# Kernel optimization log

Hardware: AMD Instinct MI355X
Metric: run time of the kernel (lower is better)

Reference implementation:

```python
import jax, jax.numpy as jnp
import numpy as np

EPS = 1e-5
NUM_HEADS = 8
TOP_K = 4

def _ln(x, s, b):
    m = x.mean(-1, keepdims=True)
    v = ((x - m) ** 2).mean(-1, keepdims=True)
    return (x - m) / jnp.sqrt(v + EPS) * s + b

def _mha(x, wq, bq, wk, bk, wv, bv, wo, bo):
    B, S, D = x.shape
    dh = D // NUM_HEADS
    q = (x @ wq + bq).reshape(B, S, NUM_HEADS, dh)
    k = (x @ wk + bk).reshape(B, S, NUM_HEADS, dh)
    v = (x @ wv + bv).reshape(B, S, NUM_HEADS, dh)
    att = jnp.einsum('bqhd,bkhd->bhqk', q, k) / np.sqrt(dh).astype(x.dtype)
    a = jax.nn.softmax(att, axis=-1)
    o = jnp.einsum('bhqk,bkhd->bqhd', a, v).reshape(B, S, D)
    return o @ wo + bo

def _moe(x, rd, ru, w1, b1, w2, b2, ws1, bs1, ws2, bs2):
    B, S, D = x.shape
    N = B * S
    E = ru.shape[-1]
    t = x.reshape(N, D)
    scores = (t @ rd) @ ru                       # [N,E] low-rank router
    probs = jax.nn.softmax(scores, axis=-1)
    tv, ti = jax.lax.top_k(probs, TOP_K)          # [N,K]
    tw = tv / tv.sum(-1, keepdims=True)           # renormalized gate weights
    oh = jax.nn.one_hot(ti, E, dtype=t.dtype)     # [N,K,E]
    gates = (oh * tw[..., None]).sum(1)           # sparse [N,E] combine weights
    h = jax.nn.gelu(jnp.einsum('nd,edh->enh', t, w1) + b1[:, None, :])
    eo = jnp.einsum('enh,ehd->end', h, w2) + b2[:, None, :]
    routed = jnp.einsum('end,ne->nd', eo, gates)
    shared = jax.nn.gelu(t @ ws1 + bs1) @ ws2 + bs2
    out = (routed + shared).reshape(B, S, D)
    # aux losses: load-balance + router z-loss
    f = oh.sum(1).mean(0)                         # mean assignments per expert
    P = probs.mean(0)
    lb = (E / TOP_K) * jnp.sum(f * P)
    z = jnp.mean(jax.nn.logsumexp(scores, axis=-1) ** 2)
    return out, lb, z

def reference(x, ln1_s, ln1_b, ln2_s, ln2_b, wq, bq, wk, bk, wv, bv, wo, bo,
              router_down, router_up, w1, b1, w2, b2, ws1, bs1, ws2, bs2, fn_s, fn_b):
    L = wq.shape[0]
    lbs, zs = [], []
    for l in range(L):
        x = x + _mha(_ln(x, ln1_s[l], ln1_b[l]), wq[l], bq[l], wk[l], bk[l],
                     wv[l], bv[l], wo[l], bo[l])
        moe_out, lb, z = _moe(_ln(x, ln2_s[l], ln2_b[l]), router_down[l], router_up[l],
                              w1[l], b1[l], w2[l], b2[l], ws1[l], bs1[l], ws2[l], bs2[l])
        x = x + moe_out
        lbs.append(lb)
        zs.append(z)
    x = _ln(x, fn_s, fn_b)
    return x, jnp.stack(lbs), jnp.stack(zs)

def setup_inputs() -> dict:
    key = jax.random.key(0)
    ks = jax.random.split(key, 16)
    L, D, E, R, H, HS, B, S = 2, 512, 32, 64, 512, 4096, 4, 1024
    w = 0.02  # init scale for weights
    return {
        'x': jax.random.normal(ks[0], (B, S, D), jnp.float32),
        'ln1_s': jnp.ones((L, D)), 'ln1_b': jnp.zeros((L, D)),
        'ln2_s': jnp.ones((L, D)), 'ln2_b': jnp.zeros((L, D)),
        'wq': jax.random.normal(ks[1], (L, D, D)) * w, 'bq': jnp.zeros((L, D)),
        'wk': jax.random.normal(ks[2], (L, D, D)) * w, 'bk': jnp.zeros((L, D)),
        'wv': jax.random.normal(ks[3], (L, D, D)) * w, 'bv': jnp.zeros((L, D)),
        'wo': jax.random.normal(ks[4], (L, D, D)) * w, 'bo': jnp.zeros((L, D)),
        'router_down': jax.random.normal(ks[5], (L, D, R)) * w,
        'router_up': jax.random.normal(ks[6], (L, R, E)) * w,
        'w1': jax.random.normal(ks[7], (L, E, D, H)) * w, 'b1': jnp.zeros((L, E, H)),
        'w2': jax.random.normal(ks[8], (L, E, H, D)) * w, 'b2': jnp.zeros((L, E, D)),
        'ws1': jax.random.normal(ks[9], (L, D, HS)) * w, 'bs1': jnp.zeros((L, HS)),
        'ws2': jax.random.normal(ks[10], (L, HS, D)) * w, 'bs2': jnp.zeros((L, D)),
        'fn_s': jnp.ones((D,)), 'fn_b': jnp.zeros((D,)),
    }
```

## Files before the change

### kernel.cpp

```cpp
#include <hip/hip_runtime.h>
#include <math.h>

#define NTOK    4096
#define DMODEL  512
#define NEXP    32
#define RRANK   64
#define HEXP    512
#define HSHARED 4096
#define SEQ     1024
#define BATCH   4
#define NHEAD   8
#define TOPK    4
#define NLAYER  2
#define QBLK    64
#define KBLK    64
#define MAXTILE 160
#define DDU     262144

typedef __attribute__((ext_vector_type(8))) short bf16x8;
typedef __attribute__((ext_vector_type(4))) float f32x4;

__device__ __forceinline__ float gelu_f(float x) {
    float t = tanhf(0.7978845608028654f * (x + 0.044715f * x * x * x));
    return 0.5f * x * (1.f + t);
}
__device__ __forceinline__ unsigned short f2bf(float f) {
    unsigned int u = __float_as_uint(f);
    u += 0x7FFFu + ((u >> 16) & 1u);
    return (unsigned short)(u >> 16);
}
__device__ __forceinline__ float bf2f(unsigned short u) {
    return __uint_as_float((unsigned int)u << 16);
}
__device__ __forceinline__ void gl_lds16(const void* g, void* l) {
    __builtin_amdgcn_global_load_lds(
        (const __attribute__((address_space(1))) void*)g,
        (__attribute__((address_space(3))) void*)l, 16, 0, 0);
}

template <int MODE>
__global__ __launch_bounds__(256) void ln_kernel(const float* __restrict__ x,
                                                 const float* __restrict__ s,
                                                 const float* __restrict__ b,
                                                 float* __restrict__ outf,
                                                 unsigned short* __restrict__ outb) {
    int wave = threadIdx.x >> 6, lane = threadIdx.x & 63;
    int row = blockIdx.x * 4 + wave;
    const float* xr = x + (size_t)row * DMODEL;
    float v[8];
    float sum = 0.f;
#pragma unroll
    for (int i = 0; i < 8; i++) { v[i] = xr[lane + i * 64]; sum += v[i]; }
#pragma unroll
    for (int o = 32; o; o >>= 1) sum += __shfl_xor(sum, o);
    float m = sum * (1.f / DMODEL);
    float vs = 0.f;
#pragma unroll
    for (int i = 0; i < 8; i++) { float d = v[i] - m; vs += d * d; }
#pragma unroll
    for (int o = 32; o; o >>= 1) vs += __shfl_xor(vs, o);
    float rstd = rsqrtf(vs * (1.f / DMODEL) + 1e-5f);
#pragma unroll
    for (int i = 0; i < 8; i++) {
        int c = lane + i * 64;
        float r = (v[i] - m) * rstd * s[c] + b[c];
        if (MODE != 1) outf[(size_t)row * DMODEL + c] = r;
        if (MODE != 0) outb[(size_t)row * DMODEL + c] = f2bf(r);
    }
}

template <int SK, bool MOE, int MODE, bool ROUTER = false>
__global__ __launch_bounds__(256) void reduceln_kernel(
    const float* __restrict__ pbuf, const float* __restrict__ bias,
    const unsigned short* __restrict__ eogb, const float* __restrict__ topw,
    const int* __restrict__ pos, float* __restrict__ xb,
    const float* __restrict__ s, const float* __restrict__ b,
    float* __restrict__ outf, unsigned short* __restrict__ outb,
    const float* __restrict__ rdru, float* __restrict__ rsc) {
    int wave = threadIdx.x >> 6, lane = threadIdx.x & 63;
    int row = blockIdx.x * 4 + wave;
    int cb = lane * 8;
    size_t base = (size_t)row * DMODEL + cb;
    float v[8];
    {
        float4 a0 = *(const float4*)(xb + base);
        float4 a1 = *(const float4*)(xb + base + 4);
        float4 b0 = *(const float4*)(bias + cb);
        float4 b1 = *(const float4*)(bias + cb + 4);
        v[0] = a0.x + b0.x; v[1] = a0.y + b0.y; v[2] = a0.z + b0.z; v[3] = a0.w + b0.w;
        v[4] = a1.x + b1.x; v[5] = a1.y + b1.y; v[6] = a1.z + b1.z; v[7] = a1.w + b1.w;
    }
#pragma unroll
    for (int sk = 0; sk < SK; sk++) {
        const float* p = pbuf + (size_t)sk * NTOK * DMODEL + base;
        float4 p0 = *(const float4*)p;
        float4 p1 = *(const float4*)(p + 4);
        v[0] += p0.x; v[1] += p0.y; v[2] += p0.z; v[3] += p0.w;
        v[4] += p1.x; v[5] += p1.y; v[6] += p1.z; v[7] += p1.w;
    }
    if (MOE) {
#pragma unroll
        for (int k = 0; k < TOPK; k++) {
            float w = topw[row * TOPK + k];
            bf16x8 e = *(const bf16x8*)(eogb + (size_t)pos[row * TOPK + k] * DMODEL + cb);
#pragma unroll
            for (int i = 0; i < 8; i++) v[i] += w * bf2f((unsigned short)e[i]);
        }
    }
    *(float4*)(xb + base) = make_float4(v[0], v[1], v[2], v[3]);
    *(float4*)(xb + base + 4) = make_float4(v[4], v[5], v[6], v[7]);
    float sum = 0.f;
#pragma unroll
    for (int i = 0; i < 8; i++) sum += v[i];
#pragma unroll
    for (int o = 32; o; o >>= 1) sum += __shfl_xor(sum, o);
    float m = sum * (1.f / DMODEL);
    float vs = 0.f;
#pragma unroll
    for (int i = 0; i < 8; i++) { float d = v[i] - m; vs += d * d; }
#pragma unroll
    for (int o = 32; o; o >>= 1) vs += __shfl_xor(vs, o);
    float rstd = rsqrtf(vs * (1.f / DMODEL) + 1e-5f);
    float rr[8];
#pragma unroll
    for (int i = 0; i < 8; i++) {
        int c = cb + i;
        rr[i] = (v[i] - m) * rstd * s[c] + b[c];
        if (MODE != 1) outf[(size_t)row * DMODEL + c] = rr[i];
        if (MODE != 0) outb[(size_t)row * DMODEL + c] = f2bf(rr[i]);
    }
    if (ROUTER) {
        float sc[NEXP];
#pragma unroll
        for (int e = 0; e < NEXP; e++) sc[e] = 0.f;
#pragma unroll
        for (int i = 0; i < 8; i++) {
            const float4* rp = (const float4*)(rdru + (size_t)(cb + i) * NEXP);
            float rv = rr[i];
#pragma unroll
            for (int e4 = 0; e4 < 8; e4++) {
                float4 q = rp[e4];
                sc[e4 * 4 + 0] += rv * q.x;
                sc[e4 * 4 + 1] += rv * q.y;
                sc[e4 * 4 + 2] += rv * q.z;
                sc[e4 * 4 + 3] += rv * q.w;
            }
        }
#pragma unroll
        for (int e = 0; e < NEXP; e++) {
#pragma unroll
            for (int o = 32; o; o >>= 1) sc[e] += __shfl_xor(sc[e], o);
        }
        if (lane == 0) {
            float* rp = rsc + (size_t)row * NEXP;
#pragma unroll
            for (int e = 0; e < NEXP; e++) rp[e] = sc[e];
        }
    }
}

__global__ __launch_bounds__(256) void wtall_kernel(
    const float* __restrict__ wq, const float* __restrict__ wk,
    const float* __restrict__ wv, const float* __restrict__ wo,
    const float* __restrict__ w1, const float* __restrict__ w2,
    const float* __restrict__ ws1, const float* __restrict__ ws2,
    const float* __restrict__ bq, const float* __restrict__ bk, const float* __restrict__ bv,
    unsigned short* __restrict__ wqkvt, unsigned short* __restrict__ wot,
    unsigned short* __restrict__ w1t, unsigned short* __restrict__ w2t,
    unsigned short* __restrict__ ws1t, unsigned short* __restrict__ ws2t,
    float* __restrict__ bqkv, int* __restrict__ stats) {
    __shared__ float tbuf[64][68];
    int bkid = blockIdx.x;
    int tid = threadIdx.x;
    if (bkid >= 5376) {
        int i = (bkid - 5376) * 256 + tid;
        float val = (i < 512) ? bq[i] : (i < 1024 ? bk[i - 512] : bv[i - 1024]);
        bqkv[i] = val;
        if (i < 160) stats[i] = 0;
        return;
    }
    const float* src;
    unsigned short* dst;
    int K, N, tx, ty;
    if (bkid < 256) {
        int w = bkid >> 6, t = bkid & 63;
        K = 512; N = 512; ty = t >> 3; tx = t & 7;
        if (w == 0)      { src = wq; dst = wqkvt; }
        else if (w == 1) { src = wk; dst = wqkvt + DDU; }
        else if (w == 2) { src = wv; dst = wqkvt + 2 * (size_t)DDU; }
        else             { src = wo; dst = wot; }
    } else if (bkid < 2304) {
        int t = bkid - 256; int e = t >> 6; int tt = t & 63;
        K = 512; N = 512; ty = tt >> 3; tx = tt & 7;
        src = w1 + (size_t)e * DDU; dst = w1t + (size_t)e * DDU;
    } else if (bkid < 4352) {
        int t = bkid - 2304; int e = t >> 6; int tt = t & 63;
        K = 512; N = 512; ty = tt >> 3; tx = tt & 7;
        src = w2 + (size_t)e * DDU; dst = w2t + (size_t)e * DDU;
    } else if (bkid < 4864) {
        int t = bkid - 4352;
        K = 512; N = 4096; tx = t & 63; ty = t >> 6;
        src = ws1; dst = ws1t;
    } else {
        int t = bkid - 4864;
        K = 4096; N = 512; tx = t & 7; ty = t >> 3;
        src = ws2; dst = ws2t;
    }
    int k0 = ty * 64, n0 = tx * 64;
    int r = tid >> 2, cb4 = (tid & 3) * 4;
#pragma unroll
    for (int i = 0; i < 4; i++)
        *(float4*)&tbuf[r][cb4 + i * 16] = *(const float4*)(src + (size_t)(k0 + r) * N + n0 + cb4 + i * 16);
    __syncthreads();
    int g = tid & 7, nr = tid >> 3;
#pragma unroll
    for (int i = 0; i < 2; i++) {
        int n = nr + i * 32;
        bf16x8 v;
#pragma unroll
        for (int j = 0; j < 8; j++) v[j] = (short)f2bf(tbuf[g * 8 + j][n]);
        *(bf16x8*)(dst + (size_t)(n0 + n) * K + k0 + g * 8) = v;
    }
}

__global__ __launch_bounds__(256) void vtr_kernel(const unsigned short* __restrict__ QKV,
                                                  unsigned short* __restrict__ Vt) {
    int st = blockIdx.x, hh = blockIdx.y, bb = blockIdx.z;
    __shared__ unsigned short t[64][72];
    int r = threadIdx.x >> 3, g = threadIdx.x & 7;
#pragma unroll
    for (int i = 0; i < 2; i++) {
        int row = r + i * 32;
        bf16x8 v = *(const bf16x8*)(QKV + (size_t)(bb * SEQ + st * 64 + row) * 1536 + 1024 + hh * 64 + g * 8);
        *(bf16x8*)&t[row][g * 8] = v;
    }
    __syncthreads();
#pragma unroll
    for (int i = 0; i < 2; i++) {
        int d = r + i * 32;
        bf16x8 v;
#pragma unroll
        for (int j = 0; j < 8; j++) v[j] = (short)t[g * 8 + j][d];
        *(bf16x8*)(Vt + (size_t)((bb * NHEAD + hh) * 64 + d) * SEQ + st * 64 + g * 8) = v;
    }
}

template <bool GELU, bool DORES, bool GATHER, bool EXPERT, bool OUTBF16, int SK = 1, int BK = 64>
__global__ __launch_bounds__(256, 2) void gemm_mfma(
    const unsigned short* __restrict__ Ab, const unsigned short* __restrict__ Wt,
    const float* __restrict__ bias, const float* __restrict__ res,
    void* __restrict__ Cvoid, int M, int Nn, int Kk,
    const int* __restrict__ rowmap, const int* __restrict__ cntp,
    const int* __restrict__ offp, const int* __restrict__ tinfo) {
    constexpr int RS  = BK * 2;
    constexpr int CH  = RS / 16;
    constexpr int RPI = 1024 / RS;
    constexpr int AIW = 32 / RPI;
    constexpr int BIW = 16 / RPI;
    unsigned int bid = blockIdx.y * gridDim.x + blockIdx.x;
    unsigned int tot = gridDim.x * gridDim.y;
    unsigned int lg = (bid & 7) * (tot >> 3) + (bid >> 3);
    unsigned int bx = lg % gridDim.x;
    unsigned int by = lg / gridDim.x;
    int n0 = bx * 64;
    int m0;
    size_t cbase = 0;
    int kbeg = 0, kend = Kk;
    if (EXPERT) {
        int t = by;
        if (t >= tinfo[0]) return;
        int e = tinfo[1 + 2 * t];
        m0 = tinfo[2 + 2 * t];
        M = cntp[e];
        Wt += (size_t)e * Nn * Kk;
        bias += (size_t)e * Nn;
        int oe = offp[e];
        cbase = (size_t)oe * Nn;
        if (GATHER) rowmap += oe;
        else Ab += (size_t)oe * Kk;
    } else {
        m0 = by * 128;
    }
    if (SK > 1) {
        int s = blockIdx.z;
        int chunk = Kk / SK;
        kbeg = s * chunk;
        kend = kbeg + chunk;
        cbase = (size_t)s * M * Nn;
    }
    __shared__ short As[128 * BK];
    __shared__ short Bs[64 * BK];
    char* asb = (char*)As;
    char* bsb = (char*)Bs;
    int tid = threadIdx.x;
    int wave = tid >> 6, lane = tid & 63;
    int wm = wave >> 1, wn = wave & 1;
    int l15 = lane & 15, l16 = lane >> 4;
    int c16 = lane & (CH - 1);
    int ro  = lane / CH;

    const char* aptr[AIW];
    const char* bptr[BIW];
#pragma unroll
    for (int j = 0; j < AIW; j++) {
        int rloc = j * RPI + ro;
        int row = wave * 32 + rloc;
        int grow = m0 + row;
        int arow = GATHER ? rowmap[grow] : grow;
        int srcoff = ((c16 ^ (rloc & (CH - 1))) << 4);
        aptr[j] = (const char*)Ab + (((size_t)arow * Kk) << 1) + srcoff;
    }
#pragma unroll
    for (int j = 0; j < BIW; j++) {
        int rloc = j * RPI + ro;
        int row = wave * 16 + rloc;
        int srcoff = ((c16 ^ (rloc & (CH - 1))) << 4);
        bptr[j] = (const char*)Wt + (((size_t)(n0 + row) * Kk) << 1) + srcoff;
    }

    f32x4 acc[4][2];
#pragma unroll
    for (int m = 0; m < 4; m++)
#pragma unroll
        for (int n = 0; n < 2; n++)
#pragma unroll
            for (int j = 0; j < 4; j++) acc[m][n][j] = 0.f;

    for (int k0 = kbeg; k0 < kend; k0 += BK) {
        size_t kb = (size_t)k0 << 1;
#pragma unroll
        for (int j = 0; j < AIW; j++) gl_lds16(aptr[j] + kb, asb + wave * 32 * RS + j * 1024);
#pragma unroll
        for (int j = 0; j < BIW; j++) gl_lds16(bptr[j] + kb, bsb + wave * 16 * RS + j * 1024);
        __syncthreads();
#pragma unroll
        for (int kk = 0; kk < BK / 32; kk++) {
            int k8 = kk * 4 + l16;
            bf16x8 a[4], b[2];
#pragma unroll
            for (int m = 0; m < 4; m++) {
                int row = wm * 64 + m * 16 + l15;
                a[m] = *(const bf16x8*)(asb + row * RS + ((k8 * 16) ^ ((row & (CH - 1)) << 4)));
            }
#pragma unroll
            for (int n = 0; n < 2; n++) {
                int row = wn * 32 + n * 16 + l15;
                b[n] = *(const bf16x8*)(bsb + row * RS + ((k8 * 16) ^ ((row & (CH - 1)) << 4)));
            }
#pragma unroll
            for (int m = 0; m < 4; m++)
#pragma unroll
                for (int n = 0; n < 2; n++)
                    acc[m][n] = __builtin_amdgcn_mfma_f32_16x16x32_bf16(a[m], b[n], acc[m][n], 0, 0, 0);
        }
        __syncthreads();
    }

#pragma unroll
    for (int m = 0; m < 4; m++) {
#pragma unroll
        for (int n = 0; n < 2; n++) {
            int col = n0 + wn * 32 + n * 16 + l15;
            float bv = (SK == 1 && bias) ? bias[col] : 0.f;
#pragma unroll
            for (int j = 0; j < 4; j++) {
                int row = m0 + wm * 64 + m * 16 + l16 * 4 + j;
                if (row >= M) continue;
                float val = acc[m][n][j] + bv;
                if (SK == 1 && GELU) val = gelu_f(val);
                if (SK == 1 && DORES) val += res[(size_t)row * Nn + col];
                if (SK == 1 && OUTBF16)
                    ((unsigned short*)Cvoid)[cbase + (size_t)row * Nn + col] = f2bf(val);
                else
                    ((float*)Cvoid)[cbase + (size_t)row * Nn + col] = val;
            }
        }
    }
}

template <bool GELU>
__global__ __launch_bounds__(256) void gemm_tile(
    const float* __restrict__ A, const float* __restrict__ W,
    float* __restrict__ C, int M, int Nn, int Kk, int lda) {
    int n0 = blockIdx.x * 64;
    int m0 = blockIdx.y * 64;
    __shared__ float Asf[16][68];
    __shared__ float Wsf[16][68];
    int tid = threadIdx.x;
    int ml = tid >> 2, kl = (tid & 3) << 2;
    bool avalid = (m0 + ml) < M;
    int arow = m0 + ml;
    const float* aptr = A + (size_t)arow * lda + kl;
    int kr = tid >> 4, nc = (tid & 15) << 2;
    bool wvalid = (n0 + nc) < Nn;
    const float* wptr = W + (size_t)kr * Nn + n0 + nc;
    int tm = (tid >> 4) << 2, tn = (tid & 15) << 2;
    float acc[4][4] = {{0.f}};
    for (int k0 = 0; k0 < Kk; k0 += 16) {
        float4 av = make_float4(0.f, 0.f, 0.f, 0.f);
        float4 wv = make_float4(0.f, 0.f, 0.f, 0.f);
        if (avalid) av = *(const float4*)(aptr + k0);
        if (wvalid) wv = *(const float4*)(wptr + (size_t)k0 * Nn);
        Asf[kl + 0][ml] = av.x; Asf[kl + 1][ml] = av.y;
        Asf[kl + 2][ml] = av.z; Asf[kl + 3][ml] = av.w;
        *(float4*)&Wsf[kr][nc] = wv;
        __syncthreads();
#pragma unroll
        for (int kk = 0; kk < 16; kk++) {
            float4 a4 = *(const float4*)&Asf[kk][tm];
            float4 w4 = *(const float4*)&Wsf[kk][tn];
            acc[0][0] += a4.x * w4.x; acc[0][1] += a4.x * w4.y; acc[0][2] += a4.x * w4.z; acc[0][3] += a4.x * w4.w;
            acc[1][0] += a4.y * w4.x; acc[1][1] += a4.y * w4.y; acc[1][2] += a4.y * w4.z; acc[1][3] += a4.y * w4.w;
            acc[2][0] += a4.z * w4.x; acc[2][1] += a4.z * w4.y; acc[2][2] += a4.z * w4.z; acc[2][3] += a4.z * w4.w;
            acc[3][0] += a4.w * w4.x; acc[3][1] += a4.w * w4.y; acc[3][2] += a4.w * w4.z; acc[3][3] += a4.w * w4.w;
        }
        __syncthreads();
    }
#pragma unroll
    for (int i = 0; i < 4; i++) {
        int mm = m0 + tm + i;
        if (mm >= M) break;
        float* crow = C + (size_t)mm * Nn;
#pragma unroll
        for (int j = 0; j < 4; j++) {
            int nn = n0 + tn + j;
            if (nn >= Nn) continue;
            float val = acc[i][j];
            if (GELU) val = gelu_f(val);
            crow[nn] = val;
        }
    }
}

__global__ __launch_bounds__(256, 2) void attn_mfma(const unsigned short* __restrict__ QKV,
                                                    const unsigned short* __restrict__ Vt,
                                                    unsigned short* __restrict__ O) {
    int qt = blockIdx.x, hh = blockIdx.y, bb = blockIdx.z;
    __shared__ char lds[32768];
    char* Qs = lds;
    char* Ks = lds + 8192;
    char* Vs = lds + 16384;
    char* Ps = lds + 24576;
    int tid = threadIdx.x;
    int w = tid >> 6, l = tid & 63;
    int l15 = l & 15, l16 = l >> 4;

    {
        int r = tid >> 3, g = tid & 7;
        const unsigned short* qbase = QKV + (size_t)(bb * SEQ + qt * QBLK) * 1536 + hh * 64;
#pragma unroll
        for (int i = 0; i < 2; i++) {
            int row = r + i * 32;
            bf16x8 v = *(const bf16x8*)(qbase + (size_t)row * 1536 + g * 8);
            *(bf16x8*)(Qs + row * 128 + ((g * 16) ^ ((row & 7) << 4))) = v;
        }
    }
    f32x4 accO[4];
#pragma unroll
    for (int n = 0; n < 4; n++)
#pragma unroll
        for (int j = 0; j < 4; j++) accO[n][j] = 0.f;
    float m_r[4] = {-1e30f, -1e30f, -1e30f, -1e30f};
    float l_r[4] = {0.f, 0.f, 0.f, 0.f};

    const unsigned short* kbase = QKV + (size_t)(bb * SEQ) * 1536 + 512 + hh * 64;
    const unsigned short* vbase = Vt + (size_t)((bb * NHEAD + hh) * 64) * SEQ;

    for (int kt = 0; kt < SEQ / KBLK; kt++) {
        __syncthreads();
        {
            int r = tid >> 3, g = tid & 7;
#pragma unroll
            for (int i = 0; i < 2; i++) {
                int row = r + i * 32;
                bf16x8 kv = *(const bf16x8*)(kbase + (size_t)(kt * KBLK + row) * 1536 + g * 8);
                *(bf16x8*)(Ks + row * 128 + ((g * 16) ^ ((row & 7) << 4))) = kv;
                bf16x8 vv = *(const bf16x8*)(vbase + (size_t)row * SEQ + kt * KBLK + g * 8);
                *(bf16x8*)(Vs + row * 128 + ((g * 16) ^ ((row & 7) << 4))) = vv;
            }
        }
        __syncthreads();
        f32x4 s_acc[4];
#pragma unroll
        for (int n = 0; n < 4; n++)
#pragma unroll
            for (int j = 0; j < 4; j++) s_acc[n][j] = 0.f;
#pragma unroll
        for (int st = 0; st < 2; st++) {
            int kb = st * 64 + l16 * 16;
            int qrow = w * 16 + l15;
            bf16x8 a = *(const bf16x8*)(Qs + qrow * 128 + (kb ^ ((qrow & 7) << 4)));
#pragma unroll
            for (int n = 0; n < 4; n++) {
                int kr = n * 16 + l15;
                bf16x8 b = *(const bf16x8*)(Ks + kr * 128 + (kb ^ ((kr & 7) << 4)));
                s_acc[n] = __builtin_amdgcn_mfma_f32_16x16x32_bf16(a, b, s_acc[n], 0, 0, 0);
            }
        }
        char* pw = Ps + w * 2048;
#pragma unroll
        for (int j = 0; j < 4; j++) {
            float s0 = s_acc[0][j] * 0.125f, s1 = s_acc[1][j] * 0.125f;
            float s2 = s_acc[2][j] * 0.125f, s3 = s_acc[3][j] * 0.125f;
            float tmax = fmaxf(fmaxf(s0, s1), fmaxf(s2, s3));
#pragma unroll
            for (int o = 1; o < 16; o <<= 1) tmax = fmaxf(tmax, __shfl_xor(tmax, o));
            float mnew = fmaxf(m_r[j], tmax);
            float resc = __expf(m_r[j] - mnew);
            float p0 = __expf(s0 - mnew), p1 = __expf(s1 - mnew);
            float p2 = __expf(s2 - mnew), p3 = __expf(s3 - mnew);
            float ps = p0 + p1 + p2 + p3;
#pragma unroll
            for (int o = 1; o < 16; o <<= 1) ps += __shfl_xor(ps, o);
            l_r[j] = l_r[j] * resc + ps;
            m_r[j] = mnew;
            accO[0][j] *= resc; accO[1][j] *= resc;
            accO[2][j] *= resc; accO[3][j] *= resc;
            int prow = l16 * 4 + j;
            int sw = (prow & 7) << 4;
            *(unsigned short*)(pw + prow * 128 + ((2 * l15) ^ sw)) = f2bf(p0);
            *(unsigned short*)(pw + prow * 128 + ((2 * l15 + 32) ^ sw)) = f2bf(p1);
            *(unsigned short*)(pw + prow * 128 + ((2 * l15 + 64) ^ sw)) = f2bf(p2);
            *(unsigned short*)(pw + prow * 128 + ((2 * l15 + 96) ^ sw)) = f2bf(p3);
        }
#pragma unroll
        for (int st = 0; st < 2; st++) {
            int kb = st * 64 + l16 * 16;
            bf16x8 pa = *(const bf16x8*)(pw + l15 * 128 + (kb ^ ((l15 & 7) << 4)));
#pragma unroll
            for (int n = 0; n < 4; n++) {
                int vr = n * 16 + l15;
                bf16x8 vb = *(const bf16x8*)(Vs + vr * 128 + (kb ^ ((vr & 7) << 4)));
                accO[n] = __builtin_amdgcn_mfma_f32_16x16x32_bf16(pa, vb, accO[n], 0, 0, 0);
            }
        }
    }
    unsigned short* obase = O + (size_t)(bb * SEQ + qt * QBLK + w * 16) * DMODEL + hh * 64;
#pragma unroll
    for (int j = 0; j < 4; j++) {
        float inv = 1.f / l_r[j];
        int row = l16 * 4 + j;
#pragma unroll
        for (int n = 0; n < 4; n++)
            obase[(size_t)row * DMODEL + n * 16 + l15] = f2bf(accO[n][j] * inv);
    }
}

__global__ __launch_bounds__(256) void router_topk(const float* __restrict__ rsc,
                                                   float* __restrict__ topw,
                                                   int* __restrict__ topi,
                                                   int* __restrict__ cnt,
                                                   float* __restrict__ sumP,
                                                   float* __restrict__ zacc) {
    __shared__ float wP[4][NEXP];
    __shared__ int wC[4][NEXP];
    __shared__ float wZ[4];
    int tid = threadIdx.x;
    int wv = tid >> 6, lane = tid & 63;
    int n = blockIdx.x * 256 + tid;
    float sc[NEXP];
    float mx = -1e30f;
#pragma unroll
    for (int e = 0; e < NEXP; e++) { sc[e] = rsc[n * NEXP + e]; mx = fmaxf(mx, sc[e]); }
    float se = 0.f;
#pragma unroll
    for (int e = 0; e < NEXP; e++) { sc[e] = expf(sc[e] - mx); se += sc[e]; }
    float invse = 1.f / se;
    float lse = mx + logf(se);
    float z = lse * lse;
#pragma unroll
    for (int o = 32; o; o >>= 1) z += __shfl_xor(z, o);
    if (lane == 0) wZ[wv] = z;
#pragma unroll
    for (int e = 0; e < NEXP; e++) {
        float pv = sc[e] * invse;
#pragma unroll
        for (int o = 32; o; o >>= 1) pv += __shfl_xor(pv, o);
        if (lane == 0) wP[wv][e] = pv;
    }
    float tv[TOPK]; int ti[TOPK];
#pragma unroll
    for (int k = 0; k < TOPK; k++) {
        float best = -1.f; int bi = 0;
#pragma unroll
        for (int e = 0; e < NEXP; e++) {
            if (sc[e] > best) { best = sc[e]; bi = e; }
        }
        tv[k] = best * invse; ti[k] = bi; sc[bi] = -1.f;
    }
    float s4 = tv[0] + tv[1] + tv[2] + tv[3];
#pragma unroll
    for (int k = 0; k < TOPK; k++) {
        topw[n * TOPK + k] = tv[k] / s4;
        topi[n * TOPK + k] = ti[k];
    }
#pragma unroll
    for (int e = 0; e < NEXP; e++) {
        unsigned long long b0 = __ballot(ti[0] == e);
        unsigned long long b1 = __ballot(ti[1] == e);
        unsigned long long b2 = __ballot(ti[2] == e);
        unsigned long long b3 = __ballot(ti[3] == e);
        if (lane == 0)
            wC[wv][e] = __popcll(b0) + __popcll(b1) + __popcll(b2) + __popcll(b3);
    }
    __syncthreads();
    if (tid < NEXP) {
        atomicAdd(&sumP[tid], wP[0][tid] + wP[1][tid] + wP[2][tid] + wP[3][tid]);
        atomicAdd(&cnt[tid], wC[0][tid] + wC[1][tid] + wC[2][tid] + wC[3][tid]);
    }
    if (tid == 0) atomicAdd(zacc, wZ[0] + wZ[1] + wZ[2] + wZ[3]);
}

__global__ void scanaux_kernel(const int* __restrict__ cnt, int* __restrict__ poff,
                               int* __restrict__ tinfo, int* __restrict__ perm,
                               const float* __restrict__ sumP, const float* __restrict__ zacc,
                               float* __restrict__ out_aux, int l) {
    int lane = threadIdx.x;
    int c = (lane < NEXP) ? cnt[lane] : 0;
    int nt = (c + 127) >> 7;
    int x = nt;
#pragma unroll
    for (int o = 1; o < 32; o <<= 1) {
        int y = __shfl_up(x, o);
        if (lane >= o) x += y;
    }
    int excl = x - nt;
    if (lane < NEXP) {
        poff[lane] = excl * 128;
        for (int i = 0; i < nt; i++) {
            tinfo[1 + 2 * (excl + i)] = lane;
            tinfo[2 + 2 * (excl + i)] = i * 128;
        }
        for (int i = c; i < nt * 128; i++) perm[excl * 128 + i] = 0;
    }
    float lb = (lane < NEXP) ? ((float)c / (float)NTOK) * (sumP[lane] / (float)NTOK) : 0.f;
#pragma unroll
    for (int o = 32; o; o >>= 1) lb += __shfl_xor(lb, o);
    if (lane == 31) {
        tinfo[0] = x;
        out_aux[l] = lb * (float)NEXP / (float)TOPK;
        out_aux[NLAYER + l] = zacc[0] / (float)NTOK;
    }
}

__global__ __launch_bounds__(256) void scatter_kernel(const int* __restrict__ topi,
                                                      const int* __restrict__ poff,
                                                      int* __restrict__ cursor,
                                                      int* __restrict__ perm,
                                                      int* __restrict__ pos) {
    __shared__ int lcnt[NEXP];
    __shared__ int lbase[NEXP];
    if (threadIdx.x < NEXP) lcnt[threadIdx.x] = 0;
    __syncthreads();
    int i = blockIdx.x * 256 + threadIdx.x;
    int e = topi[i];
    int lr = atomicAdd(&lcnt[e], 1);
    __syncthreads();
    if (threadIdx.x < NEXP && lcnt[threadIdx.x] > 0)
        lbase[threadIdx.x] = atomicAdd(&cursor[threadIdx.x], lcnt[threadIdx.x]);
    __syncthreads();
    int g = poff[e] + lbase[e] + lr;
    perm[g] = i >> 2;
    pos[i] = g;
}

extern "C" void kernel_launch(void* const* d_in, const int* in_sizes, int n_in,
                              void* d_out, int out_size, void* d_ws, size_t ws_size,
                              hipStream_t stream) {
    (void)in_sizes; (void)n_in; (void)out_size; (void)ws_size;
    const float* x_in  = (const float*)d_in[0];
    const float* ln1_s = (const float*)d_in[1];
    const float* ln1_b = (const float*)d_in[2];
    const float* ln2_s = (const float*)d_in[3];
    const float* ln2_b = (const float*)d_in[4];
    const float* wq = (const float*)d_in[5];
    const float* bq = (const float*)d_in[6];
    const float* wk = (const float*)d_in[7];
    const float* bk = (const float*)d_in[8];
    const float* wv = (const float*)d_in[9];
    const float* bv = (const float*)d_in[10];
    const float* wo = (const float*)d_in[11];
    const float* bo = (const float*)d_in[12];
    const float* rdw = (const float*)d_in[13];
    const float* ruw = (const float*)d_in[14];
    const float* w1 = (const float*)d_in[15];
    const float* b1 = (const float*)d_in[16];
    const float* w2 = (const float*)d_in[17];
    const float* b2 = (const float*)d_in[18];
    const float* ws1 = (const float*)d_in[19];
    const float* bs1 = (const float*)d_in[20];
    const float* ws2 = (const float*)d_in[21];
    const float* bs2 = (const float*)d_in[22];
    const float* fn_s = (const float*)d_in[23];
    const float* fn_b = (const float*)d_in[24];

    float* ws = (float*)d_ws;
    const size_t ND = (size_t)NTOK * DMODEL;
    const size_t PADROWS = (size_t)MAXTILE * 128;
    size_t o = 0;
    float* xb  = ws + o; o += ND;
    unsigned short* hb     = (unsigned short*)(ws + o); o += ND / 2;
    unsigned short* qkv_bf = (unsigned short*)(ws + o); o += (size_t)NTOK * 1536 / 2;
    unsigned short* vT     = (unsigned short*)(ws + o); o += ND / 2;
    unsigned short* t1b    = (unsigned short*)(ws + o); o += ND / 2;
    unsigned short* hidb   = (unsigned short*)(ws + o); o += (size_t)NTOK * HSHARED / 2;
    unsigned short* eogb   = (unsigned short*)(ws + o); o += PADROWS * DMODEL / 2;
    float* pbuf = ws + o; o += 4 * ND;
    float* rdru = ws + o; o += (size_t)DMODEL * NEXP;
    float* rsc  = ws + o; o += (size_t)NTOK * NEXP;
    float* topw = ws + o; o += (size_t)NTOK * TOPK;
    float* bqkv = ws + o; o += 1536;
    int* topi = (int*)(ws + o); o += (size_t)NTOK * TOPK;
    int* pos  = (int*)(ws + o); o += (size_t)NTOK * TOPK;
    int* perm = (int*)(ws + o); o += PADROWS;
    int* stats = (int*)(ws + o); o += 256;
    int* tinfo = (int*)(ws + o); o += 512;
    int* cnt = stats;
    int* cursor = stats + 32;
    int* poff = stats + 64;
    float* sumP = (float*)(stats + 96);
    float* zacc = sumP + 32;
    unsigned short* wbf = (unsigned short*)(ws + o);
    unsigned short* wqkvt = wbf;
    unsigned short* wot  = wqkvt + 3 * (size_t)DDU;
    unsigned short* w1t  = wot + DDU;
    unsigned short* w2t  = w1t + (size_t)NEXP * DDU;
    unsigned short* ws1t = w2t + (size_t)NEXP * DDU;
    unsigned short* ws2t = ws1t + (size_t)DMODEL * HSHARED;

    float* out_x = (float*)d_out;
    float* out_aux = out_x + ND;

    hipMemcpyAsync(xb, x_in, ND * sizeof(float), hipMemcpyDeviceToDevice, stream);

    dim3 blk(256);
    dim3 gQKV(1536 / 64, NTOK / 128);
    dim3 gOP(DMODEL / 64, NTOK / 128, 2);
    dim3 gF2(DMODEL / 64, NTOK / 128, 4);
    dim3 gHS(HSHARED / 64, NTOK / 128);
    dim3 gE1(HEXP / 64, MAXTILE);
    dim3 gE2(DMODEL / 64, MAXTILE);

    for (int l = 0; l < NLAYER; l++) {
        const size_t DD = (size_t)DMODEL * DMODEL;
        wtall_kernel<<<5382, blk, 0, stream>>>(
            wq + l * DD, wk + l * DD, wv + l * DD, wo + l * DD,
            w1 + (size_t)l * NEXP * DD, w2 + (size_t)l * NEXP * DD,
            ws1 + (size_t)l * DMODEL * HSHARED, ws2 + (size_t)l * HSHARED * DMODEL,
            bq + l * DMODEL, bk + l * DMODEL, bv + l * DMODEL,
            wqkvt, wot, w1t, w2t, ws1t, ws2t, bqkv, stats);
        gemm_tile<false><<<dim3(1, 8), blk, 0, stream>>>(
            rdw + (size_t)l * DMODEL * RRANK, ruw + (size_t)l * RRANK * NEXP, rdru, DMODEL, NEXP, RRANK, RRANK);

        if (l == 0)
            ln_kernel<1><<<NTOK / 4, blk, 0, stream>>>(xb, ln1_s, ln1_b, nullptr, hb);
        gemm_mfma<false, false, false, false, true><<<gQKV, blk, 0, stream>>>(
            hb, wqkvt, bqkv, nullptr, qkv_bf, NTOK, 1536, DMODEL, nullptr, nullptr, nullptr, nullptr);
        vtr_kernel<<<dim3(SEQ / 64, NHEAD, BATCH), blk, 0, stream>>>(qkv_bf, vT);
        attn_mfma<<<dim3(SEQ / QBLK, NHEAD, BATCH), blk, 0, stream>>>(qkv_bf, vT, t1b);
        gemm_mfma<false, false, false, false, false, 2><<<gOP, blk, 0, stream>>>(
            t1b, wot, nullptr, nullptr, pbuf, NTOK, DMODEL, DMODEL, nullptr, nullptr, nullptr, nullptr);
        reduceln_kernel<2, false, 1, true><<<NTOK / 4, blk, 0, stream>>>(
            pbuf, bo + l * DMODEL, nullptr, nullptr, nullptr, xb,
            ln2_s + l * DMODEL, ln2_b + l * DMODEL, nullptr, hb, rdru, rsc);
        router_topk<<<NTOK / 256, blk, 0, stream>>>(rsc, topw, topi, cnt, sumP, zacc);
        scanaux_kernel<<<1, 64, 0, stream>>>(cnt, poff, tinfo, perm, sumP, zacc, out_aux, l);
        scatter_kernel<<<NTOK * TOPK / 256, blk, 0, stream>>>(topi, poff, cursor, perm, pos);
        gemm_mfma<true, false, true, true, true><<<gE1, blk, 0, stream>>>(
            hb, w1t, b1 + (size_t)l * NEXP * HEXP, nullptr,
            hidb, 0, HEXP, DMODEL, perm, cnt, poff, tinfo);
        gemm_mfma<false, false, false, true, true><<<gE2, blk, 0, stream>>>(
            hidb, w2t, b2 + (size_t)l * NEXP * DMODEL, nullptr,
            eogb, 0, DMODEL, HEXP, nullptr, cnt, poff, tinfo);
        gemm_mfma<true, false, false, false, true><<<gHS, blk, 0, stream>>>(
            hb, ws1t, bs1 + (size_t)l * HSHARED, nullptr,
            hidb, NTOK, HSHARED, DMODEL, nullptr, nullptr, nullptr, nullptr);
        gemm_mfma<false, false, false, false, false, 4><<<gF2, blk, 0, stream>>>(
            hidb, ws2t, nullptr, nullptr, pbuf, NTOK, DMODEL, HSHARED, nullptr, nullptr, nullptr, nullptr);
        if (l + 1 < NLAYER) {
            reduceln_kernel<4, true, 1, false><<<NTOK / 4, blk, 0, stream>>>(
                pbuf, bs2 + l * DMODEL, eogb, topw, pos, xb,
                ln1_s + (l + 1) * DMODEL, ln1_b + (l + 1) * DMODEL, nullptr, hb, nullptr, nullptr);
        } else {
            reduceln_kernel<4, true, 0, false><<<NTOK / 4, blk, 0, stream>>>(
                pbuf, bs2 + l * DMODEL, eogb, topw, pos, xb,
                fn_s, fn_b, out_x, nullptr, nullptr, nullptr);
        }
    }
}
```

Before: 566.9 us.

## Merge shared and routed expert GEMMs into combined MLP1/MLP2 launches

Factors the MFMA GEMM into a device body and adds two kernels that each run the shared-expert GEMM and the routed-expert GEMM in one grid, split by block index. This cuts four launches per layer to two and lets the small, tile-count-dependent expert GEMMs fill the GPU alongside the large shared GEMMs, so there are fewer tail-underutilization gaps. A separate ehid buffer is added so the expert hidden activations no longer alias the shared hidden buffer. Expert blocks with no tile exit early, which can leave idle slots in the combined grid.

```diff
diff --git a/kernel.cpp b/kernel.cpp
--- a/kernel.cpp
+++ b/kernel.cpp
@@ -245,23 +245,21 @@
     }
 }
 
-template <bool GELU, bool DORES, bool GATHER, bool EXPERT, bool OUTBF16, int SK = 1, int BK = 64>
-__global__ __launch_bounds__(256, 2) void gemm_mfma(
-    const unsigned short* __restrict__ Ab, const unsigned short* __restrict__ Wt,
-    const float* __restrict__ bias, const float* __restrict__ res,
-    void* __restrict__ Cvoid, int M, int Nn, int Kk,
-    const int* __restrict__ rowmap, const int* __restrict__ cntp,
-    const int* __restrict__ offp, const int* __restrict__ tinfo) {
-    constexpr int RS  = BK * 2;
-    constexpr int CH  = RS / 16;
-    constexpr int RPI = 1024 / RS;
-    constexpr int AIW = 32 / RPI;
-    constexpr int BIW = 16 / RPI;
-    unsigned int bid = blockIdx.y * gridDim.x + blockIdx.x;
-    unsigned int tot = gridDim.x * gridDim.y;
-    unsigned int lg = (bid & 7) * (tot >> 3) + (bid >> 3);
-    unsigned int bx = lg % gridDim.x;
-    unsigned int by = lg / gridDim.x;
+template <bool GELU, bool GATHER, bool EXPERT, bool OUTBF16, int SK>
+__device__ __forceinline__ void gemm_body(
+    char* asb, char* bsb,
+    unsigned int rb, unsigned int gx, unsigned int tot, int zidx,
+    const unsigned short* Ab, const unsigned short* Wt,
+    const float* bias, void* Cvoid, int M, int Nn, int Kk,
+    const int* rowmap, const int* cntp, const int* offp, const int* tinfo) {
+    constexpr int RS  = 128;
+    constexpr int CH  = 8;
+    constexpr int RPI = 8;
+    constexpr int AIW = 4;
+    constexpr int BIW = 2;
+    unsigned int lg = (rb & 7) * (tot >> 3) + (rb >> 3);
+    unsigned int bx = lg % gx;
+    unsigned int by = lg / gx;
     int n0 = bx * 64;
     int m0;
     size_t cbase = 0;
@@ -282,16 +280,11 @@
         m0 = by * 128;
     }
     if (SK > 1) {
-        int s = blockIdx.z;
         int chunk = Kk / SK;
-        kbeg = s * chunk;
+        kbeg = zidx * chunk;
         kend = kbeg + chunk;
-        cbase = (size_t)s * M * Nn;
-    }
-    __shared__ short As[128 * BK];
-    __shared__ short Bs[64 * BK];
-    char* asb = (char*)As;
-    char* bsb = (char*)Bs;
+        cbase = (size_t)zidx * M * Nn;
+    }
     int tid = threadIdx.x;
     int wave = tid >> 6, lane = tid & 63;
     int wm = wave >> 1, wn = wave & 1;
@@ -326,7 +319,7 @@
 #pragma unroll
             for (int j = 0; j < 4; j++) acc[m][n][j] = 0.f;
 
-    for (int k0 = kbeg; k0 < kend; k0 += BK) {
+    for (int k0 = kbeg; k0 < kend; k0 += 64) {
         size_t kb = (size_t)k0 << 1;
 #pragma unroll
         for (int j = 0; j < AIW; j++) gl_lds16(aptr[j] + kb, asb + wave * 32 * RS + j * 1024);
@@ -334,7 +327,7 @@
         for (int j = 0; j < BIW; j++) gl_lds16(bptr[j] + kb, bsb + wave * 16 * RS + j * 1024);
         __syncthreads();
 #pragma unroll
-        for (int kk = 0; kk < BK / 32; kk++) {
+        for (int kk = 0; kk < 2; kk++) {
             int k8 = kk * 4 + l16;
             bf16x8 a[4], b[2];
 #pragma unroll
@@ -368,13 +361,72 @@
                 if (row >= M) continue;
                 float val = acc[m][n][j] + bv;
                 if (SK == 1 && GELU) val = gelu_f(val);
-                if (SK == 1 && DORES) val += res[(size_t)row * Nn + col];
                 if (SK == 1 && OUTBF16)
                     ((unsigned short*)Cvoid)[cbase + (size_t)row * Nn + col] = f2bf(val);
                 else
                     ((float*)Cvoid)[cbase + (size_t)row * Nn + col] = val;
             }
         }
+    }
+}
+
+template <bool GELU, bool GATHER, bool EXPERT, bool OUTBF16, int SK = 1>
+__global__ __launch_bounds__(256, 2) void gemm_mfma(
+    const unsigned short* __restrict__ Ab, const unsigned short* __restrict__ Wt,
+    const float* __restrict__ bias, void* __restrict__ Cvoid,
+    int M, int Nn, int Kk,
+    const int* __restrict__ rowmap, const int* __restrict__ cntp,
+    const int* __restrict__ offp, const int* __restrict__ tinfo) {
+    __shared__ short As[128 * 64];
+    __shared__ short Bs[64 * 64];
+    gemm_body<GELU, GATHER, EXPERT, OUTBF16, SK>(
+        (char*)As, (char*)Bs,
+        blockIdx.y * gridDim.x + blockIdx.x, gridDim.x, gridDim.x * gridDim.y, blockIdx.z,
+        Ab, Wt, bias, Cvoid, M, Nn, Kk, rowmap, cntp, offp, tinfo);
+}
+
+__global__ __launch_bounds__(256, 2) void mlp1_kernel(
+    const unsigned short* __restrict__ hb,
+    const unsigned short* __restrict__ ws1t, const float* __restrict__ bs1,
+    unsigned short* __restrict__ hidb,
+    const unsigned short* __restrict__ w1t, const float* __restrict__ b1,
+    unsigned short* __restrict__ ehid,
+    const int* __restrict__ perm, const int* __restrict__ cnt,
+    const int* __restrict__ poff, const int* __restrict__ tinfo) {
+    __shared__ short As[128 * 64];
+    __shared__ short Bs[64 * 64];
+    unsigned int bid = blockIdx.x;
+    if (bid < 2048) {
+        gemm_body<true, false, false, true, 1>(
+            (char*)As, (char*)Bs, bid, 64, 2048, 0,
+            hb, ws1t, bs1, hidb, NTOK, HSHARED, DMODEL, nullptr, nullptr, nullptr, nullptr);
+    } else {
+        gemm_body<true, true, true, true, 1>(
+            (char*)As, (char*)Bs, bid - 2048, 8, 1280, 0,
+            hb, w1t, b1, ehid, 0, HEXP, DMODEL, perm, cnt, poff, tinfo);
+    }
+}
+
+__global__ __launch_bounds__(256, 2) void mlp2_kernel(
+    const unsigned short* __restrict__ hidb,
+    const unsigned short* __restrict__ ws2t, float* __restrict__ pbuf,
+    const unsigned short* __restrict__ ehid,
+    const unsigned short* __restrict__ w2t, const float* __restrict__ b2,
+    unsigned short* __restrict__ eogb,
+    const int* __restrict__ cnt, const int* __restrict__ poff,
+    const int* __restrict__ tinfo) {
+    __shared__ short As[128 * 64];
+    __shared__ short Bs[64 * 64];
+    unsigned int bid = blockIdx.x;
+    if (bid < 1024) {
+        int zidx = bid >> 8;
+        gemm_body<false, false, false, false, 4>(
+            (char*)As, (char*)Bs, bid & 255, 8, 256, zidx,
+            hidb, ws2t, nullptr, pbuf, NTOK, DMODEL, HSHARED, nullptr, nullptr, nullptr, nullptr);
+    } else {
+        gemm_body<false, false, true, true, 1>(
+            (char*)As, (char*)Bs, bid - 1024, 8, 1280, 0,
+            ehid, w2t, b2, eogb, 0, DMODEL, HEXP, nullptr, cnt, poff, tinfo);
     }
 }
 
@@ -704,6 +756,7 @@
     unsigned short* vT     = (unsigned short*)(ws + o); o += ND / 2;
     unsigned short* t1b    = (unsigned short*)(ws + o); o += ND / 2;
     unsigned short* hidb   = (unsigned short*)(ws + o); o += (size_t)NTOK * HSHARED / 2;
+    unsigned short* ehid   = (unsigned short*)(ws + o); o += PADROWS * HEXP / 2;
     unsigned short* eogb   = (unsigned short*)(ws + o); o += PADROWS * DMODEL / 2;
     float* pbuf = ws + o; o += 4 * ND;
     float* rdru = ws + o; o += (size_t)DMODEL * NEXP;
@@ -736,10 +789,6 @@
     dim3 blk(256);
     dim3 gQKV(1536 / 64, NTOK / 128);
     dim3 gOP(DMODEL / 64, NTOK / 128, 2);
-    dim3 gF2(DMODEL / 64, NTOK / 128, 4);
-    dim3 gHS(HSHARED / 64, NTOK / 128);
-    dim3 gE1(HEXP / 64, MAXTILE);
-    dim3 gE2(DMODEL / 64, MAXTILE);
 
     for (int l = 0; l < NLAYER; l++) {
         const size_t DD = (size_t)DMODEL * DMODEL;
@@ -754,29 +803,26 @@
 
         if (l == 0)
             ln_kernel<1><<<NTOK / 4, blk, 0, stream>>>(xb, ln1_s, ln1_b, nullptr, hb);
-        gemm_mfma<false, false, false, false, true><<<gQKV, blk, 0, stream>>>(
-            hb, wqkvt, bqkv, nullptr, qkv_bf, NTOK, 1536, DMODEL, nullptr, nullptr, nullptr, nullptr);
+        gemm_mfma<false, false, false, true><<<gQKV, blk, 0, stream>>>(
+            hb, wqkvt, bqkv, qkv_bf, NTOK, 1536, DMODEL, nullptr, nullptr, nullptr, nullptr);
         vtr_kernel<<<dim3(SEQ / 64, NHEAD, BATCH), blk, 0, stream>>>(qkv_bf, vT);
         attn_mfma<<<dim3(SEQ / QBLK, NHEAD, BATCH), blk, 0, stream>>>(qkv_bf, vT, t1b);
-        gemm_mfma<false, false, false, false, false, 2><<<gOP, blk, 0, stream>>>(
-            t1b, wot, nullptr, nullptr, pbuf, NTOK, DMODEL, DMODEL, nullptr, nullptr, nullptr, nullptr);
+        gemm_mfma<false, false, false, false, 2><<<gOP, blk, 0, stream>>>(
+            t1b, wot, nullptr, pbuf, NTOK, DMODEL, DMODEL, nullptr, nullptr, nullptr, nullptr);
         reduceln_kernel<2, false, 1, true><<<NTOK / 4, blk, 0, stream>>>(
             pbuf, bo + l * DMODEL, nullptr, nullptr, nullptr, xb,
             ln2_s + l * DMODEL, ln2_b + l * DMODEL, nullptr, hb, rdru, rsc);
         router_topk<<<NTOK / 256, blk, 0, stream>>>(rsc, topw, topi, cnt, sumP, zacc);
         scanaux_kernel<<<1, 64, 0, stream>>>(cnt, poff, tinfo, perm, sumP, zacc, out_aux, l);
         scatter_kernel<<<NTOK * TOPK / 256, blk, 0, stream>>>(topi, poff, cursor, perm, pos);
-        gemm_mfma<true, false, true, true, true><<<gE1, blk, 0, stream>>>(
-            hb, w1t, b1 + (size_t)l * NEXP * HEXP, nullptr,
-            hidb, 0, HEXP, DMODEL, perm, cnt, poff, tinfo);
-        gemm_mfma<false, false, false, true, true><<<gE2, blk, 0, stream>>>(
-            hidb, w2t, b2 + (size_t)l * NEXP * DMODEL, nullptr,
-            eogb, 0, DMODEL, HEXP, nullptr, cnt, poff, tinfo);
-        gemm_mfma<true, false, false, false, true><<<gHS, blk, 0, stream>>>(
-            hb, ws1t, bs1 + (size_t)l * HSHARED, nullptr,
-            hidb, NTOK, HSHARED, DMODEL, nullptr, nullptr, nullptr, nullptr);
-        gemm_mfma<false, false, false, false, false, 4><<<gF2, blk, 0, stream>>>(
-            hidb, ws2t, nullptr, nullptr, pbuf, NTOK, DMODEL, HSHARED, nullptr, nullptr, nullptr, nullptr);
+        mlp1_kernel<<<3328, blk, 0, stream>>>(
+            hb, ws1t, bs1 + (size_t)l * HSHARED, hidb,
+            w1t, b1 + (size_t)l * NEXP * HEXP, ehid,
+            perm, cnt, poff, tinfo);
+        mlp2_kernel<<<2304, blk, 0, stream>>>(
+            hidb, ws2t, pbuf,
+            ehid, w2t, b2 + (size_t)l * NEXP * DMODEL, eogb,
+            cnt, poff, tinfo);
         if (l + 1 < NLAYER) {
             reduceln_kernel<4, true, 1, false><<<NTOK / 4, blk, 0, stream>>>(
                 pbuf, bs2 + l * DMODEL, eogb, topw, pos, xb,
```

New measurement: 533.2 us. 1.06x faster.
